# Kernel optimization log

Hardware: AMD Instinct MI355X
Metric: run time of the kernel (lower is better)

Reference implementation:

```python
import jax, jax.numpy as jnp
import numpy as np

NUM_SEGMENTS = 8192  # number of graphs in the batch (max(batch)+1 in the torch code)
EPS = 1e-10


def setup_inputs() -> dict:
    key = jax.random.key(0)
    k1, k2 = jax.random.split(key)
    N, D = 2_000_000, 32
    batch = jnp.sort(jax.random.randint(k1, (N,), 0, NUM_SEGMENTS, dtype=jnp.int64))
    x = jax.random.normal(k2, (N, D), dtype=jnp.float32)
    return {"batch": batch, "input": x}


def reference(batch, input):
    # segment-wise numerically-stable softmax over nodes sharing a batch id
    # seg_max: [S, D]; empty segments get -inf but are never gathered
    seg_max = jax.ops.segment_max(input, batch, num_segments=NUM_SEGMENTS)
    x = jnp.exp(input - seg_max[batch])            # [N, D]
    norm = jax.ops.segment_sum(x, batch, num_segments=NUM_SEGMENTS)[batch]  # [N, D]
    return x / (norm + EPS)
```

## Files before the change

### kernel.cpp

```cpp
#include <hip/hip_runtime.h>
#include <math.h>

#define NSEG 8192
#define D 32
#define EPSF 1e-10f
#define BLK 256
#define WPB 4

__global__ void init_starts_kernel(int* __restrict__ seg_start, int N) {
    int s = blockIdx.x * blockDim.x + threadIdx.x;
    if (s <= NSEG) seg_start[s] = N;
}

__global__ void find_starts_kernel(const int* __restrict__ batch,
                                   int* __restrict__ seg_start, int N) {
    int i = blockIdx.x * blockDim.x + threadIdx.x;
    if (i >= N) return;
    int b = batch[i];
    int prev = (i == 0) ? -1 : batch[i - 1];
    for (int s = prev + 1; s <= b; ++s) seg_start[s] = i;
}

typedef float v4f __attribute__((ext_vector_type(4)));

__device__ __forceinline__ v4f shfl_xor_v4(v4f v, int mask) {
    v4f r;
    r.x = __shfl_xor(v.x, mask, 64);
    r.y = __shfl_xor(v.y, mask, 64);
    r.z = __shfl_xor(v.z, mask, 64);
    r.w = __shfl_xor(v.w, mask, 64);
    return r;
}

#define ONLINE_ACC(c)                                          \
    {                                                          \
        float mn = fmaxf(m.c, v.c);                            \
        l.c = l.c * __expf(m.c - mn) + __expf(v.c - mn);       \
        m.c = mn;                                              \
    }

#define ONLINE_MERGE(c)                                        \
    {                                                          \
        float mn = fmaxf(m.c, m2.c);                           \
        l.c = l.c * __expf(m.c - mn) + l2.c * __expf(m2.c - mn); \
        m.c = mn;                                              \
    }

__global__ __launch_bounds__(BLK, 8) void seg_softmax_wave(
    const float* __restrict__ x, const int* __restrict__ seg_start,
    float* __restrict__ out)
{
    const int tid  = (int)threadIdx.x;
    const int lane = tid & 63;
    const int s    = blockIdx.x * WPB + (tid >> 6);

    const int start = seg_start[s];
    const int len   = seg_start[s + 1] - start;
    if (len <= 0) return;

    const int cg = lane & 7;
    const int rg = lane >> 3;

    const v4f* __restrict__ xin = (const v4f*)(x + (size_t)start * D);
    v4f* __restrict__       outv = (v4f*)(out + (size_t)start * D);

    const float LOW = -1e30f;
    v4f m = {LOW, LOW, LOW, LOW};
    v4f l = {0.f, 0.f, 0.f, 0.f};

    for (int r = rg; r < len; r += 8) {
        v4f v = xin[r * 8 + cg];
        ONLINE_ACC(x) ONLINE_ACC(y) ONLINE_ACC(z) ONLINE_ACC(w)
    }

    #pragma unroll
    for (int mask = 8; mask <= 32; mask <<= 1) {
        v4f m2 = shfl_xor_v4(m, mask);
        v4f l2 = shfl_xor_v4(l, mask);
        ONLINE_MERGE(x) ONLINE_MERGE(y) ONLINE_MERGE(z) ONLINE_MERGE(w)
    }

    v4f rn;
    rn.x = 1.f / (l.x + EPSF);
    rn.y = 1.f / (l.y + EPSF);
    rn.z = 1.f / (l.z + EPSF);
    rn.w = 1.f / (l.w + EPSF);

    for (int r = rg; r < len; r += 8) {
        v4f v = xin[r * 8 + cg];
        v4f e;
        e.x = __expf(v.x - m.x) * rn.x;
        e.y = __expf(v.y - m.y) * rn.y;
        e.z = __expf(v.z - m.z) * rn.z;
        e.w = __expf(v.w - m.w) * rn.w;
        __builtin_nontemporal_store(e, &outv[r * 8 + cg]);
    }
}

extern "C" void kernel_launch(void* const* d_in, const int* in_sizes, int n_in,
                              void* d_out, int out_size, void* d_ws, size_t ws_size,
                              hipStream_t stream) {
    const int*   batch = (const int*)d_in[0];
    const float* x     = (const float*)d_in[1];
    float*       out   = (float*)d_out;
    const int    N     = in_sizes[0];

    int* seg_start = (int*)d_ws;

    init_starts_kernel<<<(NSEG + 1 + 255) / 256, 256, 0, stream>>>(seg_start, N);
    find_starts_kernel<<<(N + 255) / 256, 256, 0, stream>>>(batch, seg_start, N);
    seg_softmax_wave<<<NSEG / WPB, BLK, 0, stream>>>(x, seg_start, out);
}
```

Before: 470.5 us.

## Cache segment rows in registers and use one block per segment

Each segment now gets a full 256-thread block instead of one wave. Segments of up to 320 rows are held in registers, so the input is read once instead of twice. The online-softmax exp work is replaced by a plain two-pass max then sum, with a block reduction through shared memory. Segments longer than 320 rows fall back to a loop that writes exps and rescales them in place. The cost is higher register use, lower occupancy, and extra syncthreads.

```diff
diff --git a/kernel.cpp b/kernel.cpp
--- a/kernel.cpp
+++ b/kernel.cpp
@@ -5,7 +5,7 @@
 #define D 32
 #define EPSF 1e-10f
 #define BLK 256
-#define WPB 4
+#define K_CAP 10
 
 __global__ void init_starts_kernel(int* __restrict__ seg_start, int N) {
     int s = blockIdx.x * blockDim.x + threadIdx.x;
@@ -23,6 +23,12 @@
 
 typedef float v4f __attribute__((ext_vector_type(4)));
 
+__device__ __forceinline__ v4f v4max(v4f a, v4f b) {
+    v4f r;
+    r.x = fmaxf(a.x, b.x); r.y = fmaxf(a.y, b.y);
+    r.z = fmaxf(a.z, b.z); r.w = fmaxf(a.w, b.w);
+    return r;
+}
 __device__ __forceinline__ v4f shfl_xor_v4(v4f v, int mask) {
     v4f r;
     r.x = __shfl_xor(v.x, mask, 64);
@@ -32,68 +38,121 @@
     return r;
 }
 
-#define ONLINE_ACC(c)                                          \
-    {                                                          \
-        float mn = fmaxf(m.c, v.c);                            \
-        l.c = l.c * __expf(m.c - mn) + __expf(v.c - mn);       \
-        m.c = mn;                                              \
-    }
-
-#define ONLINE_MERGE(c)                                        \
-    {                                                          \
-        float mn = fmaxf(m.c, m2.c);                           \
-        l.c = l.c * __expf(m.c - mn) + l2.c * __expf(m2.c - mn); \
-        m.c = mn;                                              \
-    }
-
-__global__ __launch_bounds__(BLK, 8) void seg_softmax_wave(
+__global__ __launch_bounds__(BLK, 5) void seg_softmax_reg(
     const float* __restrict__ x, const int* __restrict__ seg_start,
     float* __restrict__ out)
 {
-    const int tid  = (int)threadIdx.x;
-    const int lane = tid & 63;
-    const int s    = blockIdx.x * WPB + (tid >> 6);
+    __shared__ v4f red[4 * 8];
 
+    const int s     = blockIdx.x;
     const int start = seg_start[s];
     const int len   = seg_start[s + 1] - start;
     if (len <= 0) return;
 
-    const int cg = lane & 7;
-    const int rg = lane >> 3;
+    const int tid  = (int)threadIdx.x;
+    const int cg   = tid & 7;
+    const int rg   = tid >> 3;
+    const int wave = tid >> 6;
+    const int lane = tid & 63;
 
-    const v4f* __restrict__ xin = (const v4f*)(x + (size_t)start * D);
+    const v4f* __restrict__ xin  = (const v4f*)(x + (size_t)start * D);
     v4f* __restrict__       outv = (v4f*)(out + (size_t)start * D);
 
-    const float LOW = -1e30f;
-    v4f m = {LOW, LOW, LOW, LOW};
-    v4f l = {0.f, 0.f, 0.f, 0.f};
+    const v4f NEGINF = {-INFINITY, -INFINITY, -INFINITY, -INFINITY};
 
-    for (int r = rg; r < len; r += 8) {
-        v4f v = xin[r * 8 + cg];
-        ONLINE_ACC(x) ONLINE_ACC(y) ONLINE_ACC(z) ONLINE_ACC(w)
-    }
+    if (len <= 32 * K_CAP) {
+        v4f st[K_CAP];
+        #pragma unroll
+        for (int k = 0; k < K_CAP; ++k) {
+            int r = rg + 32 * k;
+            st[k] = (r < len) ? xin[r * 8 + cg] : NEGINF;
+        }
 
-    #pragma unroll
-    for (int mask = 8; mask <= 32; mask <<= 1) {
-        v4f m2 = shfl_xor_v4(m, mask);
-        v4f l2 = shfl_xor_v4(l, mask);
-        ONLINE_MERGE(x) ONLINE_MERGE(y) ONLINE_MERGE(z) ONLINE_MERGE(w)
-    }
+        v4f lmax = NEGINF;
+        #pragma unroll
+        for (int k = 0; k < K_CAP; ++k) lmax = v4max(lmax, st[k]);
+        lmax = v4max(lmax, shfl_xor_v4(lmax, 8));
+        lmax = v4max(lmax, shfl_xor_v4(lmax, 16));
+        lmax = v4max(lmax, shfl_xor_v4(lmax, 32));
+        if (lane < 8) red[wave * 8 + cg] = lmax;
+        __syncthreads();
+        v4f cmax = v4max(v4max(red[0 * 8 + cg], red[1 * 8 + cg]),
+                         v4max(red[2 * 8 + cg], red[3 * 8 + cg]));
+        __syncthreads();
 
-    v4f rn;
-    rn.x = 1.f / (l.x + EPSF);
-    rn.y = 1.f / (l.y + EPSF);
-    rn.z = 1.f / (l.z + EPSF);
-    rn.w = 1.f / (l.w + EPSF);
+        v4f lsum = {0.f, 0.f, 0.f, 0.f};
+        #pragma unroll
+        for (int k = 0; k < K_CAP; ++k) {
+            v4f e;
+            e.x = __expf(st[k].x - cmax.x);
+            e.y = __expf(st[k].y - cmax.y);
+            e.z = __expf(st[k].z - cmax.z);
+            e.w = __expf(st[k].w - cmax.w);
+            st[k] = e;
+            lsum += e;
+        }
+        lsum += shfl_xor_v4(lsum, 8);
+        lsum += shfl_xor_v4(lsum, 16);
+        lsum += shfl_xor_v4(lsum, 32);
+        if (lane < 8) red[wave * 8 + cg] = lsum;
+        __syncthreads();
+        v4f csum = (red[0 * 8 + cg] + red[1 * 8 + cg]) +
+                   (red[2 * 8 + cg] + red[3 * 8 + cg]);
+        v4f rn;
+        rn.x = 1.f / (csum.x + EPSF);
+        rn.y = 1.f / (csum.y + EPSF);
+        rn.z = 1.f / (csum.z + EPSF);
+        rn.w = 1.f / (csum.w + EPSF);
 
-    for (int r = rg; r < len; r += 8) {
-        v4f v = xin[r * 8 + cg];
-        v4f e;
-        e.x = __expf(v.x - m.x) * rn.x;
-        e.y = __expf(v.y - m.y) * rn.y;
-        e.z = __expf(v.z - m.z) * rn.z;
-        e.w = __expf(v.w - m.w) * rn.w;
-        __builtin_nontemporal_store(e, &outv[r * 8 + cg]);
+        #pragma unroll
+        for (int k = 0; k < K_CAP; ++k) {
+            int r = rg + 32 * k;
+            if (r < len) {
+                v4f e = st[k] * rn;
+                __builtin_nontemporal_store(e, &outv[r * 8 + cg]);
+            }
+        }
+    } else {
+        v4f lmax = NEGINF;
+        for (int r = rg; r < len; r += 32)
+            lmax = v4max(lmax, xin[r * 8 + cg]);
+        lmax = v4max(lmax, shfl_xor_v4(lmax, 8));
+        lmax = v4max(lmax, shfl_xor_v4(lmax, 16));
+        lmax = v4max(lmax, shfl_xor_v4(lmax, 32));
+        if (lane < 8) red[wave * 8 + cg] = lmax;
+        __syncthreads();
+        v4f cmax = v4max(v4max(red[0 * 8 + cg], red[1 * 8 + cg]),
+                         v4max(red[2 * 8 + cg], red[3 * 8 + cg]));
+        __syncthreads();
+
+        v4f lsum = {0.f, 0.f, 0.f, 0.f};
+        for (int r = rg; r < len; r += 32) {
+            v4f v = xin[r * 8 + cg];
+            v4f e;
+            e.x = __expf(v.x - cmax.x);
+            e.y = __expf(v.y - cmax.y);
+            e.z = __expf(v.z - cmax.z);
+            e.w = __expf(v.w - cmax.w);
+            outv[r * 8 + cg] = e;
+            lsum += e;
+        }
+        lsum += shfl_xor_v4(lsum, 8);
+        lsum += shfl_xor_v4(lsum, 16);
+        lsum += shfl_xor_v4(lsum, 32);
+        if (lane < 8) red[wave * 8 + cg] = lsum;
+        __syncthreads();
+        v4f csum = (red[0 * 8 + cg] + red[1 * 8 + cg]) +
+                   (red[2 * 8 + cg] + red[3 * 8 + cg]);
+        v4f rn;
+        rn.x = 1.f / (csum.x + EPSF);
+        rn.y = 1.f / (csum.y + EPSF);
+        rn.z = 1.f / (csum.z + EPSF);
+        rn.w = 1.f / (csum.w + EPSF);
+
+        for (int r = rg; r < len; r += 32) {
+            v4f e = outv[r * 8 + cg];
+            outv[r * 8 + cg] = e * rn;
+        }
     }
 }
 
@@ -109,5 +168,5 @@
 
     init_starts_kernel<<<(NSEG + 1 + 255) / 256, 256, 0, stream>>>(seg_start, N);
     find_starts_kernel<<<(N + 255) / 256, 256, 0, stream>>>(batch, seg_start, N);
-    seg_softmax_wave<<<NSEG / WPB, BLK, 0, stream>>>(x, seg_start, out);
+    seg_softmax_reg<<<NSEG, BLK, 0, stream>>>(x, seg_start, out);
 }
```

New measurement: 440.9 us. 6.3% less time.
